# Optimization experiments

Measured on AMD Instinct MI355X. Metric: run time of the kernel, lower is better.

The kernel has to match this reference:

```python
import jax, jax.numpy as jnp
import numpy as np

SOS_TOKEN = 0
VOCAB, EMBED, HIDDEN = 32000, 256, 256


def setup_inputs() -> dict:
    key = jax.random.key(0)
    ks = jax.random.split(key, 10)
    B, S, T = 32, 128, 128
    s = 0.05
    return {
        "encoder_outputs": jax.random.normal(ks[0], (B, S, HIDDEN), jnp.float32),
        "encoder_hidden": jax.random.normal(ks[1], (1, B, HIDDEN), jnp.float32),
        "target_tensor": jax.random.randint(ks[2], (B, T), 0, VOCAB),
        "embedding": jax.random.normal(ks[3], (VOCAB, EMBED), jnp.float32) * s,
        "W_ih": jax.random.normal(ks[4], (3 * HIDDEN, EMBED + HIDDEN), jnp.float32) * s,
        "W_hh": jax.random.normal(ks[5], (3 * HIDDEN, HIDDEN), jnp.float32) * s,
        "b_ih": jax.random.normal(ks[6], (3 * HIDDEN,), jnp.float32) * s,
        "b_hh": jax.random.normal(ks[7], (3 * HIDDEN,), jnp.float32) * s,
        "W_out": jax.random.normal(ks[8], (VOCAB, HIDDEN), jnp.float32) * s,
        "b_out": jax.random.normal(ks[9], (VOCAB,), jnp.float32) * s,
    }


def _decode(encoder_outputs, encoder_hidden, target_tensor, embedding,
            W_ih, W_hh, b_ih, b_hh, W_out, b_out):
    B, T = target_tensor.shape
    # full teacher forcing: decoder input at step t is target[t-1], step 0 is SOS
    dec_in = jnp.concatenate(
        [jnp.full((B, 1), SOS_TOKEN, dtype=target_tensor.dtype), target_tensor[:, :-1]], axis=1)
    emb = embedding[dec_in]                                     # (B,T,E)
    # attention: query = embedded input, key = value = encoder_outputs
    scores = jnp.einsum("bte,bse->bts", emb, encoder_outputs)   # (B,T,S)
    attn = jax.nn.softmax(scores, axis=2)
    context = jnp.einsum("bts,bsh->bth", attn, encoder_outputs)  # (B,T,H)
    x_seq = jnp.concatenate([emb, context], axis=2)             # (B,T,E+H)
    x_seq = jnp.swapaxes(x_seq, 0, 1)                           # (T,B,E+H)

    def gru_step(h, x):
        gi = x @ W_ih.T + b_ih                                  # (B,3H)
        gh = h @ W_hh.T + b_hh
        i_r, i_z, i_n = jnp.split(gi, 3, axis=1)
        h_r, h_z, h_n = jnp.split(gh, 3, axis=1)
        r = jax.nn.sigmoid(i_r + h_r)
        z = jax.nn.sigmoid(i_z + h_z)
        n = jnp.tanh(i_n + r * h_n)
        h_new = (1.0 - z) * n + z * h
        return h_new, h_new

    h0 = encoder_hidden[0]                                      # (B,H)
    _, hs = jax.lax.scan(gru_step, h0, x_seq)                   # (T,B,H)
    logits = hs @ W_out.T + b_out                               # (T,B,V)
    return jnp.swapaxes(logits, 0, 1)                           # (B,T,V)


def reference(encoder_outputs, encoder_hidden, target_tensor, embedding,
              W_ih, W_hh, b_ih, b_hh, W_out, b_out):
    return _decode(encoder_outputs, encoder_hidden, target_tensor, embedding,
                   W_ih, W_hh, b_ih, b_hh, W_out, b_out)
```

## Files before the change

### kernel.cpp

```cpp
#include <hip/hip_runtime.h>
#include <hip/hip_bf16.h>
#include <stdint.h>

typedef float  f32x4  __attribute__((ext_vector_type(4)));
typedef __bf16 bf16x8 __attribute__((ext_vector_type(8)));
typedef _Float16 h2v  __attribute__((ext_vector_type(2)));

#define B_ 32
#define S_ 128
#define T_ 128
#define H_ 256
#define E_ 256
#define V_ 32000
#define REG_K2 112
#define LDS_K2 16

__device__ __forceinline__ void gll16(const void* g, void* l) {
  __builtin_amdgcn_global_load_lds(
      (const __attribute__((address_space(1))) uint32_t*)g,
      (__attribute__((address_space(3))) uint32_t*)l,
      16, 0, 0);
}

__device__ __forceinline__ uint32_t pack_pair(float a, float b) {
  unsigned short lo = __builtin_bit_cast(unsigned short, (_Float16)a);
  unsigned short hi = __builtin_bit_cast(unsigned short, (_Float16)b);
  return (uint32_t)lo | ((uint32_t)hi << 16);
}

__device__ __forceinline__ float dot2(uint32_t w, uint32_t h, float acc) {
#if __has_builtin(__builtin_amdgcn_fdot2)
  return __builtin_amdgcn_fdot2(__builtin_bit_cast(h2v, w),
                                __builtin_bit_cast(h2v, h), acc, false);
#else
  h2v wv = __builtin_bit_cast(h2v, w);
  h2v hv = __builtin_bit_cast(h2v, h);
  return acc + (float)wv.x * (float)hv.x + (float)wv.y * (float)hv.y;
#endif
}

__global__ __launch_bounds__(256) void cvt_bf16_kernel(
    const float* __restrict__ src, __hip_bfloat16* __restrict__ dst, int n) {
  int i = (blockIdx.x * 256 + threadIdx.x) * 4;
  if (i + 3 < n) {
    float4 v = *(const float4*)(src + i);
    dst[i + 0] = __float2bfloat16(v.x);
    dst[i + 1] = __float2bfloat16(v.y);
    dst[i + 2] = __float2bfloat16(v.z);
    dst[i + 3] = __float2bfloat16(v.w);
  }
}

__global__ __launch_bounds__(256) void pack_whh(
    const float* __restrict__ Whh, uint32_t* __restrict__ Wp) {
  __shared__ float lds[32][257];
  int j0 = blockIdx.x * 32;
  int tid = threadIdx.x;
  #pragma unroll 4
  for (int i = 0; i < 32; ++i)
    lds[i][tid] = Whh[(size_t)(j0 + i) * 256 + tid];
  __syncthreads();
  #pragma unroll 4
  for (int i = 0; i < 16; ++i) {
    int e = i * 256 + tid;
    int k2 = e >> 5;
    int jj = e & 31;
    Wp[(size_t)k2 * 768 + j0 + jj] = pack_pair(lds[jj][2 * k2], lds[jj][2 * k2 + 1]);
  }
}

__global__ __launch_bounds__(256) void attn_kernel(
    const float* __restrict__ enc,
    const int*   __restrict__ tgt,
    const float* __restrict__ embt,
    float*       __restrict__ x_seq)
{
  int b   = blockIdx.x;
  int tc  = blockIdx.y;
  int tid = threadIdx.x;
  __shared__ __align__(16) float e_sh[256];
  __shared__ float attn_sh[128];
  __shared__ float red_sh[4];
  const float* encb = enc + (size_t)b * S_ * H_;

  for (int tt = 0; tt < 8; ++tt) {
    int t = tc * 8 + tt;
    int tok = (t == 0) ? 0 : tgt[b * T_ + t - 1];
    float ev = embt[(size_t)tok * E_ + tid];
    e_sh[tid] = ev;
    x_seq[(size_t)(t * B_ + b) * 512 + tid] = ev;
    __syncthreads();

    float sc = 0.f;
    if (tid < 128) {
      const float* er = encb + tid * H_;
      #pragma unroll 8
      for (int k = 0; k < 256; k += 4) {
        float4 e4 = *(const float4*)(e_sh + k);
        float4 r4 = *(const float4*)(er + k);
        sc += e4.x * r4.x; sc += e4.y * r4.y; sc += e4.z * r4.z; sc += e4.w * r4.w;
      }
      float mx = sc;
      #pragma unroll
      for (int o = 32; o > 0; o >>= 1) mx = fmaxf(mx, __shfl_xor(mx, o, 64));
      if ((tid & 63) == 0) red_sh[tid >> 6] = mx;
    }
    __syncthreads();
    float gmax = fmaxf(red_sh[0], red_sh[1]);
    float p = 0.f;
    if (tid < 128) {
      p = expf(sc - gmax);
      float s = p;
      #pragma unroll
      for (int o = 32; o > 0; o >>= 1) s += __shfl_xor(s, o, 64);
      if ((tid & 63) == 0) red_sh[2 + (tid >> 6)] = s;
    }
    __syncthreads();
    float tot = red_sh[2] + red_sh[3];
    if (tid < 128) attn_sh[tid] = p / tot;
    __syncthreads();

    float ctx = 0.f;
    #pragma unroll 4
    for (int s = 0; s < 128; ++s) ctx += attn_sh[s] * encb[s * H_ + tid];
    x_seq[(size_t)(t * B_ + b) * 512 + 256 + tid] = ctx;
    __syncthreads();
  }
}

__global__ __launch_bounds__(256) void gi_gemm(
    const float* __restrict__ X,
    const float* __restrict__ W,
    const float* __restrict__ bih,
    float*       __restrict__ gi)
{
  __shared__ float As[64][17];
  __shared__ float Bs[64][17];
  int tid = threadIdx.x;
  int n0 = blockIdx.x * 64;
  int m0 = blockIdx.y * 64;
  int tx = tid & 15, ty = tid >> 4;
  int lr = tid >> 2, lc = (tid & 3) * 4;
  float acc[16] = {};

  for (int k0 = 0; k0 < 512; k0 += 16) {
    float4 a4 = *(const float4*)(X + (size_t)(m0 + lr) * 512 + k0 + lc);
    float4 b4 = *(const float4*)(W + (size_t)(n0 + lr) * 512 + k0 + lc);
    As[lr][lc + 0] = a4.x; As[lr][lc + 1] = a4.y; As[lr][lc + 2] = a4.z; As[lr][lc + 3] = a4.w;
    Bs[lr][lc + 0] = b4.x; Bs[lr][lc + 1] = b4.y; Bs[lr][lc + 2] = b4.z; Bs[lr][lc + 3] = b4.w;
    __syncthreads();
    #pragma unroll
    for (int kk = 0; kk < 16; ++kk) {
      float ar[4], br[4];
      #pragma unroll
      for (int i = 0; i < 4; ++i) ar[i] = As[ty * 4 + i][kk];
      #pragma unroll
      for (int j = 0; j < 4; ++j) br[j] = Bs[tx * 4 + j][kk];
      #pragma unroll
      for (int i = 0; i < 4; ++i)
        #pragma unroll
        for (int j = 0; j < 4; ++j)
          acc[i * 4 + j] += ar[i] * br[j];
    }
    __syncthreads();
  }
  #pragma unroll
  for (int i = 0; i < 4; ++i) {
    int m = m0 + ty * 4 + i;
    #pragma unroll
    for (int j = 0; j < 4; ++j) {
      int n = n0 + tx * 4 + j;
      gi[(size_t)m * 768 + n] = acc[i * 4 + j] + bih[n];
    }
  }
}

__global__ __launch_bounds__(768) void gru_kernel(
    const float*    __restrict__ gi,
    const uint32_t* __restrict__ Wp,
    const float*    __restrict__ bhh,
    const float*    __restrict__ h0,
    __hip_bfloat16* __restrict__ hs)
{
  int b   = blockIdx.x;
  int tid = threadIdx.x;
  __shared__ uint32_t wl[LDS_K2 * 768];
  __shared__ __align__(16) uint32_t h2[128];
  __shared__ float sum_sh[512];
  __shared__ float hn_sh[256];
  __shared__ float in_sh[256];

  uint32_t wreg[REG_K2];
  #pragma unroll
  for (int i = 0; i < REG_K2; ++i) wreg[i] = Wp[(size_t)i * 768 + tid];
  #pragma unroll
  for (int i = 0; i < LDS_K2; ++i)
    wl[i * 768 + tid] = Wp[(size_t)(REG_K2 + i) * 768 + tid];

  float hprev = 0.f;
  if (tid < 256) {
    hprev = h0[b * 256 + tid];
    float other = __shfl_xor(hprev, 1);
    if (!(tid & 1)) h2[tid >> 1] = pack_pair(hprev, other);
  }
  float bj = bhh[tid];
  float gval = gi[(size_t)b * 768 + tid];
  __syncthreads();

  for (int t = 0; t < 128; ++t) {
    float gnext = 0.f;
    if (t < 127) gnext = gi[(size_t)((t + 1) * 32 + b) * 768 + tid];

    float a0 = 0.f, a1 = 0.f, a2 = 0.f, a3 = 0.f;
    #pragma unroll
    for (int k4 = 0; k4 < REG_K2 / 4; ++k4) {
      uint4 hh = *(const uint4*)&h2[k4 * 4];
      a0 = dot2(wreg[k4 * 4 + 0], hh.x, a0);
      a1 = dot2(wreg[k4 * 4 + 1], hh.y, a1);
      a2 = dot2(wreg[k4 * 4 + 2], hh.z, a2);
      a3 = dot2(wreg[k4 * 4 + 3], hh.w, a3);
    }
    #pragma unroll
    for (int k4 = 0; k4 < LDS_K2 / 4; ++k4) {
      uint4 hh = *(const uint4*)&h2[(REG_K2 / 4 + k4) * 4];
      a0 = dot2(wl[(k4 * 4 + 0) * 768 + tid], hh.x, a0);
      a1 = dot2(wl[(k4 * 4 + 1) * 768 + tid], hh.y, a1);
      a2 = dot2(wl[(k4 * 4 + 2) * 768 + tid], hh.z, a2);
      a3 = dot2(wl[(k4 * 4 + 3) * 768 + tid], hh.w, a3);
    }
    float tot = (a0 + a1) + (a2 + a3) + bj;
    if (tid < 512) {
      sum_sh[tid] = gval + tot;
    } else {
      hn_sh[tid - 512] = tot;
      in_sh[tid - 512] = gval;
    }
    __syncthreads();
    if (tid < 256) {
      float r = 1.f / (1.f + expf(-sum_sh[tid]));
      float z = 1.f / (1.f + expf(-sum_sh[256 + tid]));
      float n = tanhf(in_sh[tid] + r * hn_sh[tid]);
      float hn = (1.f - z) * n + z * hprev;
      hprev = hn;
      hs[(size_t)(t * 32 + b) * 256 + tid] = __float2bfloat16(hn);
      float other = __shfl_xor(hn, 1);
      if (!(tid & 1)) h2[tid >> 1] = pack_pair(hn, other);
    }
    gval = gnext;
    __syncthreads();
  }
}

__global__ __launch_bounds__(256) void logits_gemm(
    const __hip_bfloat16* __restrict__ A,
    const __hip_bfloat16* __restrict__ Bm,
    const float* __restrict__ bout,
    float* __restrict__ out)
{
  __shared__ __hip_bfloat16 sA[128 * 64];
  __shared__ __hip_bfloat16 sB[128 * 64];
  int tid = threadIdx.x;
  int n0 = blockIdx.x * 128;
  int m0 = blockIdx.y * 128;
  int lane = tid & 63;
  int wave = tid >> 6;
  int wm = (wave >> 1) * 64;
  int wn = (wave & 1) * 64;
  int srow = tid >> 3;
  int sk   = (tid & 7) * 8;
  f32x4 acc[4][4] = {};

  for (int kt = 0; kt < 256; kt += 64) {
    #pragma unroll
    for (int it = 0; it < 4; ++it) {
      int row = it * 32 + srow;
      gll16(A  + (size_t)(m0 + row) * 256 + kt + sk, &sA[row * 64 + sk]);
      gll16(Bm + (size_t)(n0 + row) * 256 + kt + sk, &sB[row * 64 + sk]);
    }
    __syncthreads();
    #pragma unroll
    for (int kk = 0; kk < 2; ++kk) {
      bf16x8 af[4], bfr[4];
      #pragma unroll
      for (int m = 0; m < 4; ++m)
        af[m] = *(const bf16x8*)&sA[(wm + m * 16 + (lane & 15)) * 64 + kk * 32 + (lane >> 4) * 8];
      #pragma unroll
      for (int n = 0; n < 4; ++n)
        bfr[n] = *(const bf16x8*)&sB[(wn + n * 16 + (lane & 15)) * 64 + kk * 32 + (lane >> 4) * 8];
      #pragma unroll
      for (int m = 0; m < 4; ++m)
        #pragma unroll
        for (int n = 0; n < 4; ++n)
          acc[m][n] = __builtin_amdgcn_mfma_f32_16x16x32_bf16(af[m], bfr[n], acc[m][n], 0, 0, 0);
    }
    __syncthreads();
  }

  #pragma unroll
  for (int n = 0; n < 4; ++n) {
    int col = n0 + wn + n * 16 + (lane & 15);
    float bv = bout[col];
    #pragma unroll
    for (int m = 0; m < 4; ++m) {
      int rbase = m0 + wm + m * 16 + (lane >> 4) * 4;
      #pragma unroll
      for (int r = 0; r < 4; ++r) {
        int row = rbase + r;
        int t  = row >> 5;
        int bb = row & 31;
        out[(size_t)(bb * 128 + t) * 32000 + col] = acc[m][n][r] + bv;
      }
    }
  }
}

extern "C" void kernel_launch(void* const* d_in, const int* in_sizes, int n_in,
                              void* d_out, int out_size, void* d_ws, size_t ws_size,
                              hipStream_t stream) {
  const float* enc  = (const float*)d_in[0];
  const float* ench = (const float*)d_in[1];
  const int*   tgt  = (const int*)d_in[2];
  const float* embt = (const float*)d_in[3];
  const float* Wih  = (const float*)d_in[4];
  const float* Whh  = (const float*)d_in[5];
  const float* bih  = (const float*)d_in[6];
  const float* bhh  = (const float*)d_in[7];
  const float* Wout = (const float*)d_in[8];
  const float* bout = (const float*)d_in[9];
  float* out = (float*)d_out;

  char* ws = (char*)d_ws;
  float* x_seq = (float*)(ws);
  float* gi    = (float*)(ws + 8388608);
  __hip_bfloat16* hs    = (__hip_bfloat16*)(ws + 20971520);
  __hip_bfloat16* woutb = (__hip_bfloat16*)(ws + 23068672);

  uint32_t* Wp = (uint32_t*)(out + ((size_t)out_size - 98304));

  cvt_bf16_kernel<<<8000, 256, 0, stream>>>(Wout, woutb, V_ * H_);
  pack_whh<<<24, 256, 0, stream>>>(Whh, Wp);
  attn_kernel<<<dim3(32, 16), 256, 0, stream>>>(enc, tgt, embt, x_seq);
  gi_gemm<<<dim3(12, 64), 256, 0, stream>>>(x_seq, Wih, bih, gi);
  gru_kernel<<<32, 768, 0, stream>>>(gi, Wp, bhh, ench, hs);
  logits_gemm<<<dim3(250, 32), 256, 0, stream>>>(hs, woutb, bout, out);
}
```

Before: 558.8 us.

## Compute all three GRU gates per thread with full register-resident weights

The GRU recurrence kernel now runs 256 threads per batch row instead of 768. Each thread keeps its r, z and n weight columns entirely in registers (384 packed values) and computes all three gate dot products itself. This removes the LDS-resident weight slice and the shared-memory exchange of gate sums between thread groups, so the elementwise gate math runs on every thread. In exchange each thread carries very high register pressure with only one wave per SIMD, which risks spills and leaves little latency hiding.

```diff
diff --git a/kernel.cpp b/kernel.cpp
--- a/kernel.cpp
+++ b/kernel.cpp
@@ -12,8 +12,6 @@
 #define H_ 256
 #define E_ 256
 #define V_ 32000
-#define REG_K2 112
-#define LDS_K2 16
 
 __device__ __forceinline__ void gll16(const void* g, void* l) {
   __builtin_amdgcn_global_load_lds(
@@ -175,7 +173,7 @@
   }
 }
 
-__global__ __launch_bounds__(768) void gru_kernel(
+__global__ __launch_bounds__(256, 1) void gru_kernel(
     const float*    __restrict__ gi,
     const uint32_t* __restrict__ Wp,
     const float*    __restrict__ bhh,
@@ -184,69 +182,70 @@
 {
   int b   = blockIdx.x;
   int tid = threadIdx.x;
-  __shared__ uint32_t wl[LDS_K2 * 768];
   __shared__ __align__(16) uint32_t h2[128];
-  __shared__ float sum_sh[512];
-  __shared__ float hn_sh[256];
-  __shared__ float in_sh[256];
-
-  uint32_t wreg[REG_K2];
-  #pragma unroll
-  for (int i = 0; i < REG_K2; ++i) wreg[i] = Wp[(size_t)i * 768 + tid];
-  #pragma unroll
-  for (int i = 0; i < LDS_K2; ++i)
-    wl[i * 768 + tid] = Wp[(size_t)(REG_K2 + i) * 768 + tid];
-
-  float hprev = 0.f;
-  if (tid < 256) {
-    hprev = h0[b * 256 + tid];
+
+  uint32_t w0[128], w1[128], w2[128];
+  #pragma unroll
+  for (int i = 0; i < 128; ++i) w0[i] = Wp[(size_t)i * 768 + tid];
+  #pragma unroll
+  for (int i = 0; i < 128; ++i) w1[i] = Wp[(size_t)i * 768 + 256 + tid];
+  #pragma unroll
+  for (int i = 0; i < 128; ++i) w2[i] = Wp[(size_t)i * 768 + 512 + tid];
+
+  float b_r = bhh[tid];
+  float b_z = bhh[256 + tid];
+  float b_n = bhh[512 + tid];
+
+  float hprev = h0[b * 256 + tid];
+  {
     float other = __shfl_xor(hprev, 1);
     if (!(tid & 1)) h2[tid >> 1] = pack_pair(hprev, other);
   }
-  float bj = bhh[tid];
-  float gval = gi[(size_t)b * 768 + tid];
+  const float* g0 = gi + (size_t)b * 768 + tid;
+  float gr = g0[0], gz = g0[256], gn = g0[512];
   __syncthreads();
 
   for (int t = 0; t < 128; ++t) {
-    float gnext = 0.f;
-    if (t < 127) gnext = gi[(size_t)((t + 1) * 32 + b) * 768 + tid];
-
-    float a0 = 0.f, a1 = 0.f, a2 = 0.f, a3 = 0.f;
-    #pragma unroll
-    for (int k4 = 0; k4 < REG_K2 / 4; ++k4) {
+    float pr = 0.f, pz = 0.f, pn = 0.f;
+    if (t < 127) {
+      const float* gp = gi + (size_t)((t + 1) * 32 + b) * 768 + tid;
+      pr = gp[0]; pz = gp[256]; pn = gp[512];
+    }
+
+    float ar0 = 0.f, ar1 = 0.f, ar2 = 0.f, ar3 = 0.f;
+    float az0 = 0.f, az1 = 0.f, az2 = 0.f, az3 = 0.f;
+    float an0 = 0.f, an1 = 0.f, an2 = 0.f, an3 = 0.f;
+    #pragma unroll
+    for (int k4 = 0; k4 < 32; ++k4) {
       uint4 hh = *(const uint4*)&h2[k4 * 4];
-      a0 = dot2(wreg[k4 * 4 + 0], hh.x, a0);
-      a1 = dot2(wreg[k4 * 4 + 1], hh.y, a1);
-      a2 = dot2(wreg[k4 * 4 + 2], hh.z, a2);
-      a3 = dot2(wreg[k4 * 4 + 3], hh.w, a3);
-    }
-    #pragma unroll
-    for (int k4 = 0; k4 < LDS_K2 / 4; ++k4) {
-      uint4 hh = *(const uint4*)&h2[(REG_K2 / 4 + k4) * 4];
-      a0 = dot2(wl[(k4 * 4 + 0) * 768 + tid], hh.x, a0);
-      a1 = dot2(wl[(k4 * 4 + 1) * 768 + tid], hh.y, a1);
-      a2 = dot2(wl[(k4 * 4 + 2) * 768 + tid], hh.z, a2);
-      a3 = dot2(wl[(k4 * 4 + 3) * 768 + tid], hh.w, a3);
-    }
-    float tot = (a0 + a1) + (a2 + a3) + bj;
-    if (tid < 512) {
-      sum_sh[tid] = gval + tot;
-    } else {
-      hn_sh[tid - 512] = tot;
-      in_sh[tid - 512] = gval;
-    }
-    __syncthreads();
-    if (tid < 256) {
-      float r = 1.f / (1.f + expf(-sum_sh[tid]));
-      float z = 1.f / (1.f + expf(-sum_sh[256 + tid]));
-      float n = tanhf(in_sh[tid] + r * hn_sh[tid]);
-      float hn = (1.f - z) * n + z * hprev;
-      hprev = hn;
-      hs[(size_t)(t * 32 + b) * 256 + tid] = __float2bfloat16(hn);
-      float other = __shfl_xor(hn, 1);
-      if (!(tid & 1)) h2[tid >> 1] = pack_pair(hn, other);
-    }
-    gval = gnext;
+      ar0 = dot2(w0[k4 * 4 + 0], hh.x, ar0);
+      az0 = dot2(w1[k4 * 4 + 0], hh.x, az0);
+      an0 = dot2(w2[k4 * 4 + 0], hh.x, an0);
+      ar1 = dot2(w0[k4 * 4 + 1], hh.y, ar1);
+      az1 = dot2(w1[k4 * 4 + 1], hh.y, az1);
+      an1 = dot2(w2[k4 * 4 + 1], hh.y, an1);
+      ar2 = dot2(w0[k4 * 4 + 2], hh.z, ar2);
+      az2 = dot2(w1[k4 * 4 + 2], hh.z, az2);
+      an2 = dot2(w2[k4 * 4 + 2], hh.z, an2);
+      ar3 = dot2(w0[k4 * 4 + 3], hh.w, ar3);
+      az3 = dot2(w1[k4 * 4 + 3], hh.w, az3);
+      an3 = dot2(w2[k4 * 4 + 3], hh.w, an3);
+    }
+    float ghr = (ar0 + ar1) + (ar2 + ar3) + b_r;
+    float ghz = (az0 + az1) + (az2 + az3) + b_z;
+    float ghn = (an0 + an1) + (an2 + an3) + b_n;
+
+    float r = 1.f / (1.f + expf(-(gr + ghr)));
+    float z = 1.f / (1.f + expf(-(gz + ghz)));
+    float n = tanhf(gn + r * ghn);
+    float hn = (1.f - z) * n + z * hprev;
+    hprev = hn;
+    hs[(size_t)(t * 32 + b) * 256 + tid] = __float2bfloat16(hn);
+
+    __syncthreads();
+    float other = __shfl_xor(hn, 1);
+    if (!(tid & 1)) h2[tid >> 1] = pack_pair(hn, other);
+    gr = pr; gz = pz; gn = pn;
     __syncthreads();
   }
 }
@@ -341,6 +340,6 @@
   pack_whh<<<24, 256, 0, stream>>>(Whh, Wp);
   attn_kernel<<<dim3(32, 16), 256, 0, stream>>>(enc, tgt, embt, x_seq);
   gi_gemm<<<dim3(12, 64), 256, 0, stream>>>(x_seq, Wih, bih, gi);
-  gru_kernel<<<32, 768, 0, stream>>>(gi, Wp, bhh, ench, hs);
+  gru_kernel<<<32, 256, 0, stream>>>(gi, Wp, bhh, ench, hs);
   logits_gemm<<<dim3(250, 32), 256, 0, stream>>>(hs, woutb, bout, out);
 }
```

New measurement: 856.5 us. 53.3% more time.
